# Optimization experiments

Measured on AMD Instinct MI355X. Metric: run time of the kernel, lower is better.

The kernel has to match this reference:

```python
import jax, jax.numpy as jnp
import numpy as np


def setup_inputs() -> dict:
    key = jax.random.key(0)
    k1, k2, k3, k4 = jax.random.split(key, 4)
    T, B, D, S = 4096, 16, 128, 256
    inputs = jax.random.normal(k1, (T, B, D), dtype=jnp.float32)
    z0 = jnp.zeros((B, S), dtype=jnp.float32)
    # parameters, initialized as in the torch module
    log_neg_a = jnp.full((S,), -0.5, dtype=jnp.float32)
    b = jax.random.normal(k2, (S, D), dtype=jnp.float32) * 0.01
    log_dt = jnp.log(jnp.full((S,), 0.05, dtype=jnp.float32))
    return {"inputs": inputs, "z0": z0, "log_neg_a": log_neg_a, "b": b, "log_dt": log_dt}


def reference(inputs, z0, log_neg_a, b, log_dt):
    # discretized diagonal SSM parameters
    a_real = -jnp.exp(jnp.clip(log_neg_a, -8.0, 4.0))            # [S]
    dt = jnp.exp(jnp.clip(log_dt, -8.0, 1.0))                    # [S]
    a_bar = jnp.exp(dt * a_real)                                 # [S]
    x = dt * a_real
    ratio = jnp.where(jnp.abs(x) < 1e-6, dt, jnp.expm1(x) / a_real)
    b_bar = ratio[:, None] * b                                   # [S, D]

    # precompute input projection for all timesteps: [T, B, S]
    ub = jnp.einsum('tbd,sd->tbs', inputs, b_bar)

    def step(z, u_t):
        z = a_bar[None, :] * z + u_t                             # [B, S]
        return z, z

    _, outs = jax.lax.scan(step, z0, ub)                          # [T, B, S]
    return outs
```

## Files before the change

### kernel.cpp

```cpp
#include <hip/hip_runtime.h>
#include <hip/hip_bf16.h>

#define T_  4096
#define B_  16
#define D_  128
#define S_  256
#define WND 64
#define C4  (T_/WND)

using bf8   = __attribute__((ext_vector_type(8))) short;
using f32x4 = __attribute__((ext_vector_type(4))) float;

__device__ inline float bfbits(unsigned short h) {
    return __builtin_bit_cast(float, (unsigned)h << 16);
}
__device__ inline unsigned short bf16bits(float f) {
    return __hip_bfloat16_raw(__float2bfloat16(f)).x;
}

__global__ __launch_bounds__(256) void k_params(
        const float* __restrict__ lna, const float* __restrict__ bmat,
        const float* __restrict__ ldt,
        float* __restrict__ abar, float* __restrict__ a64,
        __hip_bfloat16* __restrict__ bbar) {
    if (blockIdx.x < 128) {
        int idx = blockIdx.x * 256 + threadIdx.x;
        int s = idx >> 7;
        float la = fminf(fmaxf(lna[s], -8.f), 4.f);
        float ar = -expf(la);
        float lt = fminf(fmaxf(ldt[s], -8.f), 1.f);
        float dt = expf(lt);
        float xx = dt * ar;
        float ratio = (fabsf(xx) < 1e-6f) ? dt : (expm1f(xx) / ar);
        bbar[idx] = __float2bfloat16(ratio * bmat[idx]);
    } else {
        int s = threadIdx.x;
        float la = fminf(fmaxf(lna[s], -8.f), 4.f);
        float ar = -expf(la);
        float lt = fminf(fmaxf(ldt[s], -8.f), 1.f);
        float dt = expf(lt);
        float ab = expf(dt * ar);
        abar[s] = ab;
        float p = ab;
#pragma unroll
        for (int j = 0; j < 6; ++j) p *= p;
        a64[s] = p;
    }
}

__global__ __launch_bounds__(256, 4) void k_gemm(
        const float* __restrict__ x, const __hip_bfloat16* __restrict__ bbar,
        const float* __restrict__ abar,
        __hip_bfloat16* __restrict__ ub, float* __restrict__ e64) {
    const int c = blockIdx.x, b = blockIdx.y;
    __shared__ char LDS[WND * 512];
    const int tid = threadIdx.x, lane = tid & 63, w = tid >> 6;
    const int l15 = lane & 15, l4 = lane >> 4;

#pragma unroll
    for (int k = 0; k < 8; ++k) {
        int idx = tid + k * 256;
        int row = idx >> 5, seg = idx & 31;
        float4 v = *(const float4*)(x + ((size_t)(c * WND + row) * B_ + b) * D_ + seg * 4);
        __hip_bfloat162 lo = __float22bfloat162_rn(make_float2(v.x, v.y));
        __hip_bfloat162 hi = __float22bfloat162_rn(make_float2(v.z, v.w));
        uint2 pk = { *(unsigned*)&lo, *(unsigned*)&hi };
        int off = (row * 256 + seg * 8) ^ ((row & 7) << 4);
        *(uint2*)(LDS + off) = pk;
    }
    __syncthreads();

    f32x4 acc[4][4] = {};
    for (int j = 0; j < 4; ++j) {
        bf8 bfrag[4];
        int s = w * 64 + j * 16 + l15;
#pragma unroll
        for (int kk = 0; kk < 4; ++kk)
            bfrag[kk] = *(const bf8*)((const short*)bbar + s * D_ + kk * 32 + l4 * 8);
#pragma unroll
        for (int i = 0; i < 4; ++i) {
            bf8 af[4];
            int tr = i * 16 + l15;
#pragma unroll
            for (int kk = 0; kk < 4; ++kk) {
                int off = (tr * 256 + kk * 64 + l4 * 16) ^ ((tr & 7) << 4);
                af[kk] = *(const bf8*)(LDS + off);
            }
#pragma unroll
            for (int kk = 0; kk < 4; ++kk)
                acc[i][j] = __builtin_amdgcn_mfma_f32_16x16x32_bf16(
                                af[kk], bfrag[kk], acc[i][j], 0, 0, 0);
        }
    }
    __syncthreads();

#pragma unroll
    for (int j = 0; j < 4; ++j) {
        int s = w * 64 + j * 16 + l15;
        float a  = abar[s];
        float a2 = a * a, a4 = a2 * a2, a8 = a4 * a4, a16 = a8 * a8;
        float lf = (l4 == 0) ? a8 * a4 : (l4 == 1) ? a8 : (l4 == 2) ? a4 : 1.f;
        float e = 0.f;
#pragma unroll
        for (int i = 0; i < 4; ++i) {
            unsigned short h0 = bf16bits(acc[i][j][0]);
            unsigned short h1 = bf16bits(acc[i][j][1]);
            unsigned short h2 = bf16bits(acc[i][j][2]);
            unsigned short h3 = bf16bits(acc[i][j][3]);
            float inner = bfbits(h0);
            inner = fmaf(inner, a, bfbits(h1));
            inner = fmaf(inner, a, bfbits(h2));
            inner = fmaf(inner, a, bfbits(h3));
            e = fmaf(e, a16, inner);
            int row0 = i * 16 + l4 * 4;
            *(unsigned short*)(LDS + (((row0    ) * 512 + s * 2) ^ (l4 << 5))) = h0;
            *(unsigned short*)(LDS + (((row0 + 1) * 512 + s * 2) ^ (l4 << 5))) = h1;
            *(unsigned short*)(LDS + (((row0 + 2) * 512 + s * 2) ^ (l4 << 5))) = h2;
            *(unsigned short*)(LDS + (((row0 + 3) * 512 + s * 2) ^ (l4 << 5))) = h3;
        }
        e *= lf;
        e += __shfl_xor(e, 16);
        e += __shfl_xor(e, 32);
        if (l4 == 0) e64[((size_t)c * B_ + b) * S_ + s] = e;
    }
    __syncthreads();

    char* op = (char*)(ub + ((size_t)b * T_ + c * WND) * S_);
#pragma unroll
    for (int k = 0; k < 8; ++k) {
        int o = k * 4096 + tid * 16;
        int swz = (2 * k + (w >> 1)) & 3;
        uint4 v = *(uint4*)(LDS + (o ^ (swz << 5)));
        *(uint4*)(op + o) = v;
    }
}

__global__ __launch_bounds__(256) void k_scan(
        const __hip_bfloat16* __restrict__ ub, const float* __restrict__ e64,
        const float* __restrict__ abar, const float* __restrict__ a64,
        const float* __restrict__ z0, float* __restrict__ out) {
    const int c = blockIdx.x, g = blockIdx.y;
    const int w = threadIdx.x >> 6, lane = threadIdx.x & 63;
    const int b = g * 2 + (w >> 1);
    const int s0 = (w & 1) * 128 + lane * 2;

    float2 a  = *(const float2*)(abar + s0);
    float2 aw = *(const float2*)(a64 + s0);
    float2 z  = *(const float2*)(z0 + b * S_ + s0);

#pragma unroll
    for (int cp0 = 0; cp0 < C4; cp0 += 16) {
        float2 ev[16];
#pragma unroll
        for (int k = 0; k < 16; ++k)
            ev[k] = *(const float2*)(e64 + ((size_t)(cp0 + k) * B_ + b) * S_ + s0);
#pragma unroll
        for (int k = 0; k < 16; ++k) {
            float zx = fmaf(aw.x, z.x, ev[k].x);
            float zy = fmaf(aw.y, z.y, ev[k].y);
            bool p = (cp0 + k) < c;
            z.x = p ? zx : z.x;
            z.y = p ? zy : z.y;
        }
    }

    const char* up = (const char*)(ub + ((size_t)b * T_ + c * WND) * S_ + s0);
    float* op = out + ((size_t)(c * WND) * B_ + b) * S_ + s0;
#pragma unroll 8
    for (int t = 0; t < WND; ++t) {
        ushort2 v = *(const ushort2*)up;
        z.x = fmaf(a.x, z.x, bfbits(v.x));
        z.y = fmaf(a.y, z.y, bfbits(v.y));
        *(float2*)op = z;
        up += S_ * 2;
        op += (size_t)B_ * S_;
    }
}

extern "C" void kernel_launch(void* const* d_in, const int* in_sizes, int n_in,
                              void* d_out, int out_size, void* d_ws, size_t ws_size,
                              hipStream_t stream) {
    const float* x   = (const float*)d_in[0];
    const float* z0  = (const float*)d_in[1];
    const float* lna = (const float*)d_in[2];
    const float* bm  = (const float*)d_in[3];
    const float* ldt = (const float*)d_in[4];
    float* out = (float*)d_out;

    char* ws = (char*)d_ws;
    float*          abar = (float*)ws;
    float*          a64  = (float*)(ws + 4096);
    __hip_bfloat16* bbar = (__hip_bfloat16*)(ws + 8192);
    float*          e64  = (float*)(ws + (128 << 10));
    __hip_bfloat16* ub   = (__hip_bfloat16*)(ws + (4 << 20));

    k_params<<<129, 256, 0, stream>>>(lna, bm, ldt, abar, a64, bbar);
    k_gemm<<<dim3(C4, B_), 256, 0, stream>>>(x, bbar, abar, ub, e64);
    k_scan<<<dim3(C4, B_ / 2), 256, 0, stream>>>(ub, e64, abar, a64, z0, out);
}
```

Measured before the change: 48.78 us.

## Load GEMM A-fragments directly from global and use per-wave LDS staging

The GEMM kernel now loads x straight from global memory into MFMA A-fragment registers instead of staging it through shared memory, which removes two block-wide barriers. Each wave keeps its own LDS slice for the bf16 output transpose, so waves no longer synchronise with each other. The scan kernel's output writes become nontemporal stores to avoid polluting the cache. In exchange, register pressure rises (16 A fragments held per wave), global reads of x are duplicated across the four waves, and the per-wave output writes are narrower 128-byte rows.

```diff
diff --git a/kernel.cpp b/kernel.cpp
--- a/kernel.cpp
+++ b/kernel.cpp
@@ -16,6 +16,15 @@
 }
 __device__ inline unsigned short bf16bits(float f) {
     return __hip_bfloat16_raw(__float2bfloat16(f)).x;
+}
+__device__ inline bf8 cvt8(float4 v0, float4 v1) {
+    __hip_bfloat162 p0 = __float22bfloat162_rn(make_float2(v0.x, v0.y));
+    __hip_bfloat162 p1 = __float22bfloat162_rn(make_float2(v0.z, v0.w));
+    __hip_bfloat162 p2 = __float22bfloat162_rn(make_float2(v1.x, v1.y));
+    __hip_bfloat162 p3 = __float22bfloat162_rn(make_float2(v1.z, v1.w));
+    uint4 uu = make_uint4(*(unsigned*)&p0, *(unsigned*)&p1,
+                          *(unsigned*)&p2, *(unsigned*)&p3);
+    return __builtin_bit_cast(bf8, uu);
 }
 
 __global__ __launch_bounds__(256) void k_params(
@@ -53,85 +62,74 @@
         const float* __restrict__ abar,
         __hip_bfloat16* __restrict__ ub, float* __restrict__ e64) {
     const int c = blockIdx.x, b = blockIdx.y;
-    __shared__ char LDS[WND * 512];
+    __shared__ char LDS[4 * 8192];
     const int tid = threadIdx.x, lane = tid & 63, w = tid >> 6;
     const int l15 = lane & 15, l4 = lane >> 4;
+    char* myP = LDS + w * 8192;
+
+    bf8 af[4][4];
+#pragma unroll
+    for (int i = 0; i < 4; ++i) {
+        const float* xp = x + ((size_t)(c * WND + i * 16 + l15) * B_ + b) * D_ + l4 * 8;
+#pragma unroll
+        for (int kk = 0; kk < 4; ++kk) {
+            float4 v0 = *(const float4*)(xp + kk * 32);
+            float4 v1 = *(const float4*)(xp + kk * 32 + 4);
+            af[i][kk] = cvt8(v0, v1);
+        }
+    }
 
 #pragma unroll
-    for (int k = 0; k < 8; ++k) {
-        int idx = tid + k * 256;
-        int row = idx >> 5, seg = idx & 31;
-        float4 v = *(const float4*)(x + ((size_t)(c * WND + row) * B_ + b) * D_ + seg * 4);
-        __hip_bfloat162 lo = __float22bfloat162_rn(make_float2(v.x, v.y));
-        __hip_bfloat162 hi = __float22bfloat162_rn(make_float2(v.z, v.w));
-        uint2 pk = { *(unsigned*)&lo, *(unsigned*)&hi };
-        int off = (row * 256 + seg * 8) ^ ((row & 7) << 4);
-        *(uint2*)(LDS + off) = pk;
-    }
-    __syncthreads();
-
-    f32x4 acc[4][4] = {};
     for (int j = 0; j < 4; ++j) {
+        int sl = j * 16 + l15;
+        int s  = w * 64 + sl;
         bf8 bfrag[4];
-        int s = w * 64 + j * 16 + l15;
 #pragma unroll
         for (int kk = 0; kk < 4; ++kk)
             bfrag[kk] = *(const bf8*)((const short*)bbar + s * D_ + kk * 32 + l4 * 8);
+
+        f32x4 acc[4] = {};
 #pragma unroll
-        for (int i = 0; i < 4; ++i) {
-            bf8 af[4];
-            int tr = i * 16 + l15;
-#pragma unroll
-            for (int kk = 0; kk < 4; ++kk) {
-                int off = (tr * 256 + kk * 64 + l4 * 16) ^ ((tr & 7) << 4);
-                af[kk] = *(const bf8*)(LDS + off);
-            }
+        for (int i = 0; i < 4; ++i)
 #pragma unroll
             for (int kk = 0; kk < 4; ++kk)
-                acc[i][j] = __builtin_amdgcn_mfma_f32_16x16x32_bf16(
-                                af[kk], bfrag[kk], acc[i][j], 0, 0, 0);
-        }
-    }
-    __syncthreads();
+                acc[i] = __builtin_amdgcn_mfma_f32_16x16x32_bf16(
+                             af[i][kk], bfrag[kk], acc[i], 0, 0, 0);
 
-#pragma unroll
-    for (int j = 0; j < 4; ++j) {
-        int s = w * 64 + j * 16 + l15;
         float a  = abar[s];
         float a2 = a * a, a4 = a2 * a2, a8 = a4 * a4, a16 = a8 * a8;
         float lf = (l4 == 0) ? a8 * a4 : (l4 == 1) ? a8 : (l4 == 2) ? a4 : 1.f;
         float e = 0.f;
 #pragma unroll
         for (int i = 0; i < 4; ++i) {
-            unsigned short h0 = bf16bits(acc[i][j][0]);
-            unsigned short h1 = bf16bits(acc[i][j][1]);
-            unsigned short h2 = bf16bits(acc[i][j][2]);
-            unsigned short h3 = bf16bits(acc[i][j][3]);
+            unsigned short h0 = bf16bits(acc[i][0]);
+            unsigned short h1 = bf16bits(acc[i][1]);
+            unsigned short h2 = bf16bits(acc[i][2]);
+            unsigned short h3 = bf16bits(acc[i][3]);
             float inner = bfbits(h0);
             inner = fmaf(inner, a, bfbits(h1));
             inner = fmaf(inner, a, bfbits(h2));
             inner = fmaf(inner, a, bfbits(h3));
             e = fmaf(e, a16, inner);
-            int row0 = i * 16 + l4 * 4;
-            *(unsigned short*)(LDS + (((row0    ) * 512 + s * 2) ^ (l4 << 5))) = h0;
-            *(unsigned short*)(LDS + (((row0 + 1) * 512 + s * 2) ^ (l4 << 5))) = h1;
-            *(unsigned short*)(LDS + (((row0 + 2) * 512 + s * 2) ^ (l4 << 5))) = h2;
-            *(unsigned short*)(LDS + (((row0 + 3) * 512 + s * 2) ^ (l4 << 5))) = h3;
+            int base = ((i * 16 + l4 * 4) * 128 + sl * 2) ^ (l4 << 5);
+            *(unsigned short*)(myP + base      ) = h0;
+            *(unsigned short*)(myP + base + 128) = h1;
+            *(unsigned short*)(myP + base + 256) = h2;
+            *(unsigned short*)(myP + base + 384) = h3;
         }
         e *= lf;
         e += __shfl_xor(e, 16);
         e += __shfl_xor(e, 32);
         if (l4 == 0) e64[((size_t)c * B_ + b) * S_ + s] = e;
     }
-    __syncthreads();
 
-    char* op = (char*)(ub + ((size_t)b * T_ + c * WND) * S_);
+    char* gp = (char*)ub + ((size_t)b * T_ + c * WND) * 512 + w * 128;
+    const int lrow = lane >> 3, lo = (lane & 7) * 16;
 #pragma unroll
     for (int k = 0; k < 8; ++k) {
-        int o = k * 4096 + tid * 16;
-        int swz = (2 * k + (w >> 1)) & 3;
-        uint4 v = *(uint4*)(LDS + (o ^ (swz << 5)));
-        *(uint4*)(op + o) = v;
+        int row = k * 8 + lrow;
+        uint4 v = *(uint4*)(myP + row * 128 + (lo ^ (((row >> 2) & 3) << 5)));
+        *(uint4*)(gp + (size_t)row * 512 + lo) = v;
     }
 }
 
@@ -171,7 +169,8 @@
         ushort2 v = *(const ushort2*)up;
         z.x = fmaf(a.x, z.x, bfbits(v.x));
         z.y = fmaf(a.y, z.y, bfbits(v.y));
-        *(float2*)op = z;
+        __builtin_nontemporal_store(z.x, op);
+        __builtin_nontemporal_store(z.y, op + 1);
         up += S_ * 2;
         op += (size_t)B_ * S_;
     }
```

After: 57.73 us. +18.4%, slower.
